# Optimization experiments

Measured on AMD Instinct MI355X. Metric: run time of the kernel, lower is better.

## Reference

```python
import jax, jax.numpy as jnp
import numpy as np

B, N = 64, 4096          # batch of diagrams, points per diagram
H, W = 64, 64            # persistence-image resolution
L, R = 5, 256            # num_landscapes, landscape resolution
EPS = 1e-8


def setup_inputs() -> dict:
    key = jax.random.key(0)
    k1, = jax.random.split(key, 1)
    u = jax.random.uniform(k1, (B, N, 2), dtype=jnp.float32)
    birth = u[..., 0] * 0.5                      # births in [0, 0.5]
    death = birth + u[..., 1] * 0.5 + 1e-3       # deaths > births, in range
    pairs = jnp.stack([birth, death], axis=-1)   # (B, N, 2)
    sigma = jnp.float32(0.1)                     # learned bandwidth (nn.Parameter)
    return {"pairs": pairs, "sigma": sigma}


def reference(pairs, sigma):
    # ---- Persistence image (batched, vectorized over points) ----
    grid_x = jnp.linspace(0.0, 1.0, W, dtype=pairs.dtype)   # birth axis
    grid_y = jnp.linspace(0.0, 1.0, H, dtype=pairs.dtype)   # persistence axis
    birth = pairs[..., 0]                 # (B, N)
    death = pairs[..., 1]                 # (B, N)
    pers = death - birth                  # (B, N)
    # normalization per config ranges (0,1): divide by (range + 1e-8)
    birth_n = birth / (1.0 + EPS)
    pers_n = pers / (1.0 + EPS)
    weights = pers                        # weight_fn == 'linear'
    inv2s2 = 1.0 / (2.0 * sigma * sigma)
    # separable Gaussian factors: (B, N, W) and (B, N, H)
    gx = jnp.exp(-(grid_x[None, None, :] - birth_n[..., None]) ** 2 * inv2s2)
    gy = jnp.exp(-(grid_y[None, None, :] - pers_n[..., None]) ** 2 * inv2s2)
    # sum_n wt_n * gy_n(h) * gx_n(w)  ->  (B, H, W)
    image = jnp.einsum('bnh,bnw->bhw', gy * weights[..., None], gx)
    image = image / (jnp.max(image, axis=(1, 2), keepdims=True) + EPS)

    # ---- Persistence landscapes ----
    min_b = jnp.min(birth, axis=1, keepdims=True)   # (B, 1)
    max_d = jnp.max(death, axis=1, keepdims=True)   # (B, 1)
    frac = jnp.linspace(0.0, 1.0, R, dtype=pairs.dtype)
    t = min_b + (max_d - min_b) * frac[None, :]     # (B, R)
    rising = jnp.clip(t[:, None, :] - birth[..., None], 0.0)   # (B, N, R)
    falling = jnp.clip(death[..., None] - t[:, None, :], 0.0)  # (B, N, R)
    tents = jnp.minimum(rising, falling)                        # (B, N, R)
    # descending sort over points + take top L == top_k over point axis
    top = jax.lax.top_k(jnp.swapaxes(tents, 1, 2), L)[0]        # (B, R, L)
    landscapes = jnp.swapaxes(top, 1, 2)                        # (B, L, R)
    return image, landscapes
```

## Files before the change

### kernel.cpp

```cpp
#include <hip/hip_runtime.h>
#include <math.h>


#define B_   64
#define N_   4096
#define HW_  64
#define RES_ 256
#define EPSF 1e-8f
#define KC_  8
#define CPB  512
#define KP   64
#define LPB_ 16
#define LCH  64

typedef short short8v  __attribute__((ext_vector_type(8)));
typedef float float4v  __attribute__((ext_vector_type(4)));

__device__ __forceinline__ unsigned pk_bf(float a, float b) {
    unsigned ua = __float_as_uint(a), ub = __float_as_uint(b);
    return ((ua + 0x8000u) >> 16) | ((ub + 0x8000u) & 0xffff0000u);
}

#define INS5(v0, v1, v2, v3, v4, x)                       \
    {                                                     \
        float _p0 = v0, _p1 = v1, _p2 = v2, _p3 = v3;     \
        v0 = fmaxf(_p0, x);                               \
        v1 = __builtin_amdgcn_fmed3f(_p0, _p1, x);        \
        v2 = __builtin_amdgcn_fmed3f(_p1, _p2, x);        \
        v3 = __builtin_amdgcn_fmed3f(_p2, _p3, x);        \
        v4 = __builtin_amdgcn_fmed3f(_p3, v4, x);         \
    }

union SmemU {
    struct {
        unsigned short gy[64 * 72];
        unsigned short gx[64 * 72];
    } img;
    struct {
        float lmerge[4 * 5 * RES_];
        float red[8];
    } land;
};

__global__ __launch_bounds__(256) void k_partial(const float* __restrict__ pairs,
                                                 const float* __restrict__ sigp,
                                                 float* __restrict__ part,
                                                 float* __restrict__ lp) {
    __shared__ SmemU sm;
    int tid = threadIdx.x;
    int l = tid & 63, w = tid >> 6;
    int role = blockIdx.x % 3;
    int id   = blockIdx.x / 3;

    if (role == 0) {
        int kc = id & 7, b = id >> 3;
        float sigma = sigp[0];
        float ncc2 = -(0.5f / (sigma * sigma)) * 1.4426950408889634f;

        int c  = tid & 63;
        int pg = tid >> 6;
        float xc = (float)c * (1.0f / 63.0f);

        float4v acc[4];
        #pragma unroll
        for (int c4 = 0; c4 < 4; ++c4) acc[c4] = (float4v){0.f, 0.f, 0.f, 0.f};

        int rowA = (w * 16 + (l & 15)) * 72 + (l >> 4) * 8;
        const float4* pb4 = (const float4*)(pairs + 2 * ((size_t)b * N_ + kc * CPB));

        for (int ch = 0; ch < CPB / KP; ++ch) {
            int p0 = ch * 32 + pg * 8;
            unsigned gxp[8], gyp[8];
            #pragma unroll
            for (int jp = 0; jp < 8; ++jp) {
                float4 q = pb4[p0 + jp];
                float pe0 = q.y - q.x, pe1 = q.w - q.z;
                float dx0 = xc - q.x, dx1 = xc - q.z;
                float dy0 = xc - pe0, dy1 = xc - pe1;
                float ex0 = __builtin_amdgcn_exp2f(dx0 * dx0 * ncc2);
                float ex1 = __builtin_amdgcn_exp2f(dx1 * dx1 * ncc2);
                float ey0 = pe0 * __builtin_amdgcn_exp2f(dy0 * dy0 * ncc2);
                float ey1 = pe1 * __builtin_amdgcn_exp2f(dy1 * dy1 * ncc2);
                gxp[jp] = pk_bf(ex0, ex1);
                gyp[jp] = pk_bf(ey0, ey1);
            }
            __syncthreads();
            *(uint4*)&sm.img.gy[c * 72 + pg * 16]     = *(uint4*)&gyp[0];
            *(uint4*)&sm.img.gy[c * 72 + pg * 16 + 8] = *(uint4*)&gyp[4];
            *(uint4*)&sm.img.gx[c * 72 + pg * 16]     = *(uint4*)&gxp[0];
            *(uint4*)&sm.img.gx[c * 72 + pg * 16 + 8] = *(uint4*)&gxp[4];
            __syncthreads();
            #pragma unroll
            for (int ks = 0; ks < 2; ++ks) {
                short8v af = *(const short8v*)&sm.img.gy[rowA + ks * 32];
                #pragma unroll
                for (int c4 = 0; c4 < 4; ++c4) {
                    short8v bf = *(const short8v*)
                        &sm.img.gx[(c4 * 16 + (l & 15)) * 72 + ks * 32 + (l >> 4) * 8];
                    acc[c4] = __builtin_amdgcn_mfma_f32_16x16x32_bf16(af, bf, acc[c4], 0, 0, 0);
                }
            }
        }

        float* dst = part + (size_t)(b * KC_ + kc) * (HW_ * HW_);
        #pragma unroll
        for (int c4 = 0; c4 < 4; ++c4)
            #pragma unroll
            for (int reg = 0; reg < 4; ++reg) {
                int h = w * 16 + (l >> 4) * 4 + reg;
                int wv = c4 * 16 + (l & 15);
                dst[h * HW_ + wv] = acc[c4][reg];
            }
    } else {
        int idx = id * 2 + (role - 1);
        int b = idx >> 4, pcb = idx & 15;

        const float4* pb4 = (const float4*)(pairs + 2 * (size_t)b * N_);
        float mn = 1e30f, mx = -1e30f;
        #pragma unroll
        for (int i = 0; i < 8; ++i) {
            float4 q = pb4[tid + i * 256];
            mn = fminf(mn, fminf(q.x, q.z));
            mx = fmaxf(mx, fmaxf(q.y, q.w));
        }
        #pragma unroll
        for (int off = 32; off > 0; off >>= 1) {
            mn = fminf(mn, __shfl_xor(mn, off, 64));
            mx = fmaxf(mx, __shfl_xor(mx, off, 64));
        }
        if ((tid & 63) == 0) { sm.land.red[w] = mn; sm.land.red[4 + w] = mx; }
        __syncthreads();
        float minb = fminf(fminf(sm.land.red[0], sm.land.red[1]),
                           fminf(sm.land.red[2], sm.land.red[3]));
        float maxd = fmaxf(fmaxf(sm.land.red[4], sm.land.red[5]),
                           fmaxf(sm.land.red[6], sm.land.red[7]));

        int pc = pcb * 4 + w;
        float scl = (maxd - minb) * (1.0f / 255.0f);
        float t0 = minb + scl * (float)l;
        float t1 = t0 + scl * 64.0f;
        float t2 = t0 + scl * 128.0f;
        float t3 = t0 + scl * 192.0f;

        float a0 = 0.f, a1 = 0.f, a2 = 0.f, a3 = 0.f, a4 = 0.f;
        float b0 = 0.f, b1 = 0.f, b2 = 0.f, b3 = 0.f, b4 = 0.f;
        float c0 = 0.f, c1 = 0.f, c2 = 0.f, c3 = 0.f, c4 = 0.f;
        float d0 = 0.f, d1 = 0.f, d2 = 0.f, d3 = 0.f, d4 = 0.f;

        const float4* pw = (const float4*)(pairs + 2 * ((size_t)b * N_ + pc * LCH));
        #pragma unroll 4
        for (int p = 0; p < LCH / 2; ++p) {
            float4 q = pw[p];
            {
                float bb = q.x, dd = q.y;
                float x;
                x = fminf(t0 - bb, dd - t0); INS5(a0, a1, a2, a3, a4, x);
                x = fminf(t1 - bb, dd - t1); INS5(b0, b1, b2, b3, b4, x);
                x = fminf(t2 - bb, dd - t2); INS5(c0, c1, c2, c3, c4, x);
                x = fminf(t3 - bb, dd - t3); INS5(d0, d1, d2, d3, d4, x);
            }
            {
                float bb = q.z, dd = q.w;
                float x;
                x = fminf(t0 - bb, dd - t0); INS5(a0, a1, a2, a3, a4, x);
                x = fminf(t1 - bb, dd - t1); INS5(b0, b1, b2, b3, b4, x);
                x = fminf(t2 - bb, dd - t2); INS5(c0, c1, c2, c3, c4, x);
                x = fminf(t3 - bb, dd - t3); INS5(d0, d1, d2, d3, d4, x);
            }
        }

        float* lm = sm.land.lmerge;
        lm[(w * 5 + 0) * RES_ + l]       = a0; lm[(w * 5 + 1) * RES_ + l]       = a1;
        lm[(w * 5 + 2) * RES_ + l]       = a2; lm[(w * 5 + 3) * RES_ + l]       = a3;
        lm[(w * 5 + 4) * RES_ + l]       = a4;
        lm[(w * 5 + 0) * RES_ + l + 64]  = b0; lm[(w * 5 + 1) * RES_ + l + 64]  = b1;
        lm[(w * 5 + 2) * RES_ + l + 64]  = b2; lm[(w * 5 + 3) * RES_ + l + 64]  = b3;
        lm[(w * 5 + 4) * RES_ + l + 64]  = b4;
        lm[(w * 5 + 0) * RES_ + l + 128] = c0; lm[(w * 5 + 1) * RES_ + l + 128] = c1;
        lm[(w * 5 + 2) * RES_ + l + 128] = c2; lm[(w * 5 + 3) * RES_ + l + 128] = c3;
        lm[(w * 5 + 4) * RES_ + l + 128] = c4;
        lm[(w * 5 + 0) * RES_ + l + 192] = d0; lm[(w * 5 + 1) * RES_ + l + 192] = d1;
        lm[(w * 5 + 2) * RES_ + l + 192] = d2; lm[(w * 5 + 3) * RES_ + l + 192] = d3;
        lm[(w * 5 + 4) * RES_ + l + 192] = d4;
        __syncthreads();

        float v0 = lm[0 * RES_ + tid], v1 = lm[1 * RES_ + tid], v2 = lm[2 * RES_ + tid],
              v3 = lm[3 * RES_ + tid], v4 = lm[4 * RES_ + tid];
        #pragma unroll
        for (int wv = 1; wv < 4; ++wv)
            #pragma unroll
            for (int lvl = 0; lvl < 5; ++lvl) {
                float x = lm[(wv * 5 + lvl) * RES_ + tid];
                INS5(v0, v1, v2, v3, v4, x);
            }
        float* dl = lp + (size_t)(b * LPB_ + pcb) * 5 * RES_;
        dl[0 * RES_ + tid] = v0; dl[1 * RES_ + tid] = v1; dl[2 * RES_ + tid] = v2;
        dl[3 * RES_ + tid] = v3; dl[4 * RES_ + tid] = v4;
    }
}

__global__ __launch_bounds__(256) void k_finish(const float* __restrict__ part,
                                                const float* __restrict__ lp,
                                                float* __restrict__ out) {
    __shared__ float redf[4];
    int tid = threadIdx.x;
    if (blockIdx.x < 64) {
        int b = blockIdx.x;
        const float4* p0 = (const float4*)(part + (size_t)b * KC_ * (HW_ * HW_));
        float4 s[4];
        float m = 0.0f;
        #pragma unroll
        for (int i = 0; i < 4; ++i) {
            int pix4 = tid + i * 256;
            float4 v = p0[pix4];
            #pragma unroll
            for (int k2 = 1; k2 < KC_; ++k2) {
                float4 u = p0[(size_t)k2 * 1024 + pix4];
                v.x += u.x; v.y += u.y; v.z += u.z; v.w += u.w;
            }
            s[i] = v;
            m = fmaxf(m, fmaxf(fmaxf(v.x, v.y), fmaxf(v.z, v.w)));
        }
        #pragma unroll
        for (int off = 32; off > 0; off >>= 1) m = fmaxf(m, __shfl_xor(m, off, 64));
        if ((tid & 63) == 0) redf[tid >> 6] = m;
        __syncthreads();
        m = fmaxf(fmaxf(redf[0], redf[1]), fmaxf(redf[2], redf[3]));
        float inv = 1.0f / (m + EPSF);
        float4* od = (float4*)(out + (size_t)b * (HW_ * HW_));
        #pragma unroll
        for (int i = 0; i < 4; ++i) {
            float4 v = s[i];
            v.x *= inv; v.y *= inv; v.z *= inv; v.w *= inv;
            od[tid + i * 256] = v;
        }
    } else {
        int b = blockIdx.x - 64;
        const float* lpb = lp + (size_t)b * LPB_ * 5 * RES_;
        float u0 = lpb[0 * RES_ + tid], u1 = lpb[1 * RES_ + tid],
              u2 = lpb[2 * RES_ + tid], u3 = lpb[3 * RES_ + tid],
              u4 = lpb[4 * RES_ + tid];
        for (int p2 = 1; p2 < LPB_; ++p2) {
            #pragma unroll
            for (int lvl = 0; lvl < 5; ++lvl) {
                float x = lpb[(p2 * 5 + lvl) * RES_ + tid];
                INS5(u0, u1, u2, u3, u4, x);
            }
        }
        float* o = out + (size_t)B_ * HW_ * HW_ + (size_t)b * (5 * RES_);
        o[tid]            = u0;
        o[RES_ + tid]     = u1;
        o[2 * RES_ + tid] = u2;
        o[3 * RES_ + tid] = u3;
        o[4 * RES_ + tid] = u4;
    }
}

extern "C" void kernel_launch(void* const* d_in, const int* in_sizes, int n_in,
                              void* d_out, int out_size, void* d_ws, size_t ws_size,
                              hipStream_t stream) {
    const float* pairs = (const float*)d_in[0];
    const float* sig   = (const float*)d_in[1];
    float* out = (float*)d_out;
    float* wsf = (float*)d_ws;

    float* part = wsf;
    float* lp   = part + (size_t)B_ * KC_ * HW_ * HW_;

    k_partial<<<1536, 256, 0, stream>>>(pairs, sig, part, lp);
    k_finish<<<128, 256, 0, stream>>>(part, lp, out);
}
```

Before: 98.33 us.

## Skip non-overlapping diagram points per wave in landscape top-5 pass

The landscape blocks now assign each wave a contiguous 64-sample slice of t, and each thread covers one t value. Points are streamed from a 512-point chunk, and any point whose [birth, death] interval misses the wave's t range is skipped with a wave-uniform comparison on the float bit patterns. This removes the shared-memory merge across waves and cuts landscape blocks from 1024 to 512, so k_partial launches 1024 blocks instead of 1536. The savings depend on how many intervals overlap each slice of t, and the inner loop now carries branches.

```diff
diff --git a/kernel.cpp b/kernel.cpp
--- a/kernel.cpp
+++ b/kernel.cpp
@@ -9,9 +9,7 @@
 #define EPSF 1e-8f
 #define KC_  8
 #define CPB  512
-#define KP   64
-#define LPB_ 16
-#define LCH  64
+#define LPC_ 8
 
 typedef short short8v  __attribute__((ext_vector_type(8)));
 typedef float float4v  __attribute__((ext_vector_type(4)));
@@ -37,7 +35,6 @@
         unsigned short gx[64 * 72];
     } img;
     struct {
-        float lmerge[4 * 5 * RES_];
         float red[8];
     } land;
 };
@@ -48,17 +45,17 @@
                                                  float* __restrict__ lp) {
     __shared__ SmemU sm;
     int tid = threadIdx.x;
-    int l = tid & 63, w = tid >> 6;
-    int role = blockIdx.x % 3;
-    int id   = blockIdx.x / 3;
+    int l = tid & 63;
+    int w = __builtin_amdgcn_readfirstlane(tid >> 6);
+    int role = blockIdx.x & 1;
+    int id   = blockIdx.x >> 1;
 
     if (role == 0) {
         int kc = id & 7, b = id >> 3;
         float sigma = sigp[0];
         float ncc2 = -(0.5f / (sigma * sigma)) * 1.4426950408889634f;
 
-        int c  = tid & 63;
-        int pg = tid >> 6;
+        int c = tid & 63;
         float xc = (float)c * (1.0f / 63.0f);
 
         float4v acc[4];
@@ -68,8 +65,8 @@
         int rowA = (w * 16 + (l & 15)) * 72 + (l >> 4) * 8;
         const float4* pb4 = (const float4*)(pairs + 2 * ((size_t)b * N_ + kc * CPB));
 
-        for (int ch = 0; ch < CPB / KP; ++ch) {
-            int p0 = ch * 32 + pg * 8;
+        for (int ch = 0; ch < CPB / 64; ++ch) {
+            int p0 = ch * 32 + w * 8;
             unsigned gxp[8], gyp[8];
             #pragma unroll
             for (int jp = 0; jp < 8; ++jp) {
@@ -85,10 +82,10 @@
                 gyp[jp] = pk_bf(ey0, ey1);
             }
             __syncthreads();
-            *(uint4*)&sm.img.gy[c * 72 + pg * 16]     = *(uint4*)&gyp[0];
-            *(uint4*)&sm.img.gy[c * 72 + pg * 16 + 8] = *(uint4*)&gyp[4];
-            *(uint4*)&sm.img.gx[c * 72 + pg * 16]     = *(uint4*)&gxp[0];
-            *(uint4*)&sm.img.gx[c * 72 + pg * 16 + 8] = *(uint4*)&gxp[4];
+            *(uint4*)&sm.img.gy[c * 72 + w * 16]     = *(uint4*)&gyp[0];
+            *(uint4*)&sm.img.gy[c * 72 + w * 16 + 8] = *(uint4*)&gyp[4];
+            *(uint4*)&sm.img.gx[c * 72 + w * 16]     = *(uint4*)&gxp[0];
+            *(uint4*)&sm.img.gx[c * 72 + w * 16 + 8] = *(uint4*)&gxp[4];
             __syncthreads();
             #pragma unroll
             for (int ks = 0; ks < 2; ++ks) {
@@ -112,8 +109,7 @@
                 dst[h * HW_ + wv] = acc[c4][reg];
             }
     } else {
-        int idx = id * 2 + (role - 1);
-        int b = idx >> 4, pcb = idx & 15;
+        int pc = id & 7, b = id >> 3;
 
         const float4* pb4 = (const float4*)(pairs + 2 * (size_t)b * N_);
         float mn = 1e30f, mx = -1e30f;
@@ -135,67 +131,34 @@
         float maxd = fmaxf(fmaxf(sm.land.red[4], sm.land.red[5]),
                            fmaxf(sm.land.red[6], sm.land.red[7]));
 
-        int pc = pcb * 4 + w;
-        float scl = (maxd - minb) * (1.0f / 255.0f);
-        float t0 = minb + scl * (float)l;
-        float t1 = t0 + scl * 64.0f;
-        float t2 = t0 + scl * 128.0f;
-        float t3 = t0 + scl * 192.0f;
-
-        float a0 = 0.f, a1 = 0.f, a2 = 0.f, a3 = 0.f, a4 = 0.f;
-        float b0 = 0.f, b1 = 0.f, b2 = 0.f, b3 = 0.f, b4 = 0.f;
-        float c0 = 0.f, c1 = 0.f, c2 = 0.f, c3 = 0.f, c4 = 0.f;
-        float d0 = 0.f, d1 = 0.f, d2 = 0.f, d3 = 0.f, d4 = 0.f;
-
-        const float4* pw = (const float4*)(pairs + 2 * ((size_t)b * N_ + pc * LCH));
-        #pragma unroll 4
-        for (int p = 0; p < LCH / 2; ++p) {
+        float sc = (maxd - minb) * (1.0f / 255.0f);
+        float t  = minb + sc * (float)(w * 64 + l);
+        float tlo_f = minb + sc * (float)(w * 64);
+        float thi_f = minb + sc * (float)(w * 64 + 63);
+        int itlo = __builtin_amdgcn_readfirstlane(__float_as_int(tlo_f));
+        int ithi = __builtin_amdgcn_readfirstlane(__float_as_int(thi_f));
+
+        float v0 = 0.f, v1 = 0.f, v2 = 0.f, v3 = 0.f, v4 = 0.f;
+        const float4* pw = (const float4*)(pairs + 2 * ((size_t)b * N_ + pc * 512));
+        #pragma unroll 2
+        for (int p = 0; p < 256; ++p) {
             float4 q = pw[p];
-            {
-                float bb = q.x, dd = q.y;
-                float x;
-                x = fminf(t0 - bb, dd - t0); INS5(a0, a1, a2, a3, a4, x);
-                x = fminf(t1 - bb, dd - t1); INS5(b0, b1, b2, b3, b4, x);
-                x = fminf(t2 - bb, dd - t2); INS5(c0, c1, c2, c3, c4, x);
-                x = fminf(t3 - bb, dd - t3); INS5(d0, d1, d2, d3, d4, x);
-            }
-            {
-                float bb = q.z, dd = q.w;
-                float x;
-                x = fminf(t0 - bb, dd - t0); INS5(a0, a1, a2, a3, a4, x);
-                x = fminf(t1 - bb, dd - t1); INS5(b0, b1, b2, b3, b4, x);
-                x = fminf(t2 - bb, dd - t2); INS5(c0, c1, c2, c3, c4, x);
-                x = fminf(t3 - bb, dd - t3); INS5(d0, d1, d2, d3, d4, x);
-            }
-        }
-
-        float* lm = sm.land.lmerge;
-        lm[(w * 5 + 0) * RES_ + l]       = a0; lm[(w * 5 + 1) * RES_ + l]       = a1;
-        lm[(w * 5 + 2) * RES_ + l]       = a2; lm[(w * 5 + 3) * RES_ + l]       = a3;
-        lm[(w * 5 + 4) * RES_ + l]       = a4;
-        lm[(w * 5 + 0) * RES_ + l + 64]  = b0; lm[(w * 5 + 1) * RES_ + l + 64]  = b1;
-        lm[(w * 5 + 2) * RES_ + l + 64]  = b2; lm[(w * 5 + 3) * RES_ + l + 64]  = b3;
-        lm[(w * 5 + 4) * RES_ + l + 64]  = b4;
-        lm[(w * 5 + 0) * RES_ + l + 128] = c0; lm[(w * 5 + 1) * RES_ + l + 128] = c1;
-        lm[(w * 5 + 2) * RES_ + l + 128] = c2; lm[(w * 5 + 3) * RES_ + l + 128] = c3;
-        lm[(w * 5 + 4) * RES_ + l + 128] = c4;
-        lm[(w * 5 + 0) * RES_ + l + 192] = d0; lm[(w * 5 + 1) * RES_ + l + 192] = d1;
-        lm[(w * 5 + 2) * RES_ + l + 192] = d2; lm[(w * 5 + 3) * RES_ + l + 192] = d3;
-        lm[(w * 5 + 4) * RES_ + l + 192] = d4;
-        __syncthreads();
-
-        float v0 = lm[0 * RES_ + tid], v1 = lm[1 * RES_ + tid], v2 = lm[2 * RES_ + tid],
-              v3 = lm[3 * RES_ + tid], v4 = lm[4 * RES_ + tid];
-        #pragma unroll
-        for (int wv = 1; wv < 4; ++wv)
-            #pragma unroll
-            for (int lvl = 0; lvl < 5; ++lvl) {
-                float x = lm[(wv * 5 + lvl) * RES_ + tid];
+            if (__float_as_int(q.y) > itlo && __float_as_int(q.x) < ithi) {
+                float x = fminf(t - q.x, q.y - t);
                 INS5(v0, v1, v2, v3, v4, x);
             }
-        float* dl = lp + (size_t)(b * LPB_ + pcb) * 5 * RES_;
-        dl[0 * RES_ + tid] = v0; dl[1 * RES_ + tid] = v1; dl[2 * RES_ + tid] = v2;
-        dl[3 * RES_ + tid] = v3; dl[4 * RES_ + tid] = v4;
+            if (__float_as_int(q.w) > itlo && __float_as_int(q.z) < ithi) {
+                float x = fminf(t - q.z, q.w - t);
+                INS5(v0, v1, v2, v3, v4, x);
+            }
+        }
+
+        float* dl = lp + ((size_t)((b * LPC_ + pc) * 4 + w)) * 320;
+        dl[0 * 64 + l] = v0;
+        dl[1 * 64 + l] = v1;
+        dl[2 * 64 + l] = v2;
+        dl[3 * 64 + l] = v3;
+        dl[4 * 64 + l] = v4;
     }
 }
 
@@ -236,14 +199,15 @@
         }
     } else {
         int b = blockIdx.x - 64;
-        const float* lpb = lp + (size_t)b * LPB_ * 5 * RES_;
-        float u0 = lpb[0 * RES_ + tid], u1 = lpb[1 * RES_ + tid],
-              u2 = lpb[2 * RES_ + tid], u3 = lpb[3 * RES_ + tid],
-              u4 = lpb[4 * RES_ + tid];
-        for (int p2 = 1; p2 < LPB_; ++p2) {
+        int wq = tid >> 6, l = tid & 63;
+        const float* lpb = lp + (size_t)b * (LPC_ * 4 * 320) + wq * 320 + l;
+        float u0 = lpb[0 * 64], u1 = lpb[1 * 64], u2 = lpb[2 * 64],
+              u3 = lpb[3 * 64], u4 = lpb[4 * 64];
+        for (int p2 = 1; p2 < LPC_; ++p2) {
+            const float* s2 = lpb + (size_t)p2 * 4 * 320;
             #pragma unroll
             for (int lvl = 0; lvl < 5; ++lvl) {
-                float x = lpb[(p2 * 5 + lvl) * RES_ + tid];
+                float x = s2[lvl * 64];
                 INS5(u0, u1, u2, u3, u4, x);
             }
         }
@@ -267,6 +231,6 @@
     float* part = wsf;
     float* lp   = part + (size_t)B_ * KC_ * HW_ * HW_;
 
-    k_partial<<<1536, 256, 0, stream>>>(pairs, sig, part, lp);
+    k_partial<<<1024, 256, 0, stream>>>(pairs, sig, part, lp);
     k_finish<<<128, 256, 0, stream>>>(part, lp, out);
 }
```

Result: slower. 105.0 us (+6.8%).
